# Optimization experiments

Hardware: AMD Instinct MI355X
Metric: run time of the kernel (lower is better)

The kernel has to match this reference:

```python
import jax, jax.numpy as jnp
import numpy as np

B, S, E, A = 4, 2048, 1024, 1024

def setup_inputs() -> dict:
    key = jax.random.key(0)
    ks = jax.random.split(key, 6)
    scale = 1.0 / np.sqrt(E)
    return {
        "query": jax.random.normal(ks[0], (B, S, E), jnp.float32),
        "key": jax.random.normal(ks[1], (B, S, E), jnp.float32),
        "value": jax.random.normal(ks[2], (B, S, E), jnp.float32),
        "Wq": jax.random.normal(ks[3], (E, A), jnp.float32) * scale,
        "bq": jnp.zeros((A,), jnp.float32),
        "Wk": jax.random.normal(ks[4], (E, A), jnp.float32) * scale,
        "bk": jnp.zeros((A,), jnp.float32),
        "Wv": jax.random.normal(ks[5], (E, A), jnp.float32) * scale,
        "bv": jnp.zeros((A,), jnp.float32),
    }

def reference(query, key, value, Wq, bq, Wk, bk, Wv, bv):
    # QKV linear projections: [B,S,E] @ [E,A] + [A]
    q = jnp.einsum("bse,ea->bsa", query, Wq) + bq
    k = jnp.einsum("bse,ea->bsa", key, Wk) + bk
    v = jnp.einsum("bse,ea->bsa", value, Wv) + bv
    # scaled dot-product attention (no mask, single head)
    inv_sqrt_d = 1.0 / jnp.sqrt(jnp.asarray(A, q.dtype))
    scores = jnp.einsum("bqa,bka->bqk", q, k) * inv_sqrt_d  # [B,S,S]
    probs = jax.nn.softmax(scores, axis=-1)
    return jnp.einsum("bqk,bka->bqa", probs, v)
```

## Files before the change

### kernel.cpp

```cpp
#include <hip/hip_runtime.h>

typedef unsigned short u16;
typedef __attribute__((ext_vector_type(4))) float f32x4;
typedef __attribute__((ext_vector_type(8))) short s16x8;
typedef __attribute__((ext_vector_type(8))) unsigned short u16x8;
typedef __attribute__((ext_vector_type(4))) unsigned short u16x4;

__device__ __forceinline__ u16 f2b(float x) {
  union { float f; unsigned u; } v; v.f = x;
  unsigned r = v.u + 0x7fffu + ((v.u >> 16) & 1u);
  return (u16)(r >> 16);
}
__device__ __forceinline__ float b2f(u16 x) {
  union { unsigned u; float f; } v; v.u = ((unsigned)x) << 16;
  return v.f;
}

__global__ __launch_bounds__(256) void cast3_f32_bf16(const float* __restrict__ s0,
                                                      const float* __restrict__ s1,
                                                      const float* __restrict__ s2,
                                                      u16* __restrict__ dst, long n4) {
  const float* src = (blockIdx.y == 0) ? s0 : ((blockIdx.y == 1) ? s1 : s2);
  long i = blockIdx.x * 256 + threadIdx.x;
  if (i >= n4) return;
  float4 f = ((const float4*)src)[i];
  u16x4 o;
  o.x = f2b(f.x); o.y = f2b(f.y); o.z = f2b(f.z); o.w = f2b(f.w);
  ((u16x4*)(dst + blockIdx.y * n4 * 4))[i] = o;
}

__global__ __launch_bounds__(256) void transpose_cast_w3(const float* __restrict__ w0,
                                                         const float* __restrict__ w1,
                                                         const float* __restrict__ w2,
                                                         u16* __restrict__ Wt, int E_, int A_) {
  __shared__ float tile[32][33];
  const float* W = (blockIdx.z == 0) ? w0 : ((blockIdx.z == 1) ? w1 : w2);
  u16* dst = Wt + (long)blockIdx.z * E_ * A_;
  int a0 = blockIdx.x * 32, e0 = blockIdx.y * 32;
  int tx = threadIdx.x & 31, ty = threadIdx.x >> 5;
  for (int i = ty; i < 32; i += 8) tile[i][tx] = W[(long)(e0 + i) * A_ + a0 + tx];
  __syncthreads();
  for (int i = ty; i < 32; i += 8) dst[(long)(a0 + i) * E_ + e0 + tx] = f2b(tile[tx][i]);
}

template<bool OUT_BF16>
__global__ __launch_bounds__(512, 2)
void gemm256(const u16* __restrict__ Ag, const u16* __restrict__ Bg,
             const float* __restrict__ b0, const float* __restrict__ b1,
             const float* __restrict__ b2, void* __restrict__ Cg,
             int gm, int K, int N, float scale,
             long sA, long sB, long sC,
             u16* __restrict__ VtG, long vtB, int vtS) {
  __shared__ u16 lds[65536];
  char* ldsc = (char*)lds;
  const int t = threadIdx.x;
  const int w = t >> 6, l = t & 63;
  const int wm = w >> 2, wn = w & 3;

  const int nwg = gridDim.x;
  const int Lb = blockIdx.x;
  const int chunk = nwg >> 3;
  const int id = (Lb & 7) * chunk + (Lb >> 3);
  const int im = id % gm, in = id / gm;
  const int m0 = im * 256, n0 = in * 256;
  const int z = blockIdx.z;
  const float* bias = (z == 0) ? b0 : ((z == 1) ? b1 : b2);

  const u16* Ab = Ag + (long)z * sA + (long)m0 * K;
  const u16* Bb = Bg + (long)z * sB + (long)n0 * K;

  const long so0 = (long)(w * 8 + (l >> 3)) * K + (long)(((l & 7) ^ (l >> 3)) << 3);
  const int ldst0 = w << 10;

  const int cb0 = ((l >> 4) ^ (l & 7)) << 4;
  const int arow = (l & 15) << 7;
  const int aoff0 = (wm << 14) + arow + cb0;
  const int aoff1 = aoff0 ^ 64;
  const int boff0 = 32768 + ((wn >> 1) << 14) + ((wn & 1) << 13) + arow + cb0;
  const int boff1 = boff0 ^ 64;

  f32x4 acc[8][4] = {};
  s16x8 af[4][2], bf[2][2];
  const int NT = K >> 6;
  const int NT2 = NT >> 1;

#define STG2(AB, KT) do {                                                                    \
    const u16* _sp = ((AB) ? Bb : Ab) + ((long)(KT) << 6) + so0;                             \
    const int _lo = (((KT) & 1) << 16) + ((AB) << 15) + ldst0;                               \
    _Pragma("unroll") for (int _h = 0; _h < 4; ++_h)                                         \
      __builtin_amdgcn_global_load_lds(                                                      \
          (const __attribute__((address_space(1))) unsigned int*)(_sp + (long)_h * 64 * K),  \
          (__attribute__((address_space(3))) unsigned int*)(ldsc + _lo + _h * 8192),         \
          16, 0, 0);                                                                         \
  } while (0)

#define PHASE(BUF, MH, NH, RDA_, RDB_, SAB, SKT, VMN) do {                                   \
    if (RDA_) {                                                                              \
      _Pragma("unroll") for (int i = 0; i < 4; ++i) {                                        \
        af[i][0] = *(const s16x8*)(ldsc + ((BUF) << 16) + ((MH) << 13) + (i << 11) + aoff0); \
        af[i][1] = *(const s16x8*)(ldsc + ((BUF) << 16) + ((MH) << 13) + (i << 11) + aoff1); \
      }                                                                                      \
    }                                                                                        \
    if (RDB_) {                                                                              \
      _Pragma("unroll") for (int j = 0; j < 2; ++j) {                                        \
        bf[j][0] = *(const s16x8*)(ldsc + ((BUF) << 16) + ((NH) << 12) + (j << 11) + boff0); \
        bf[j][1] = *(const s16x8*)(ldsc + ((BUF) << 16) + ((NH) << 12) + (j << 11) + boff1); \
      }                                                                                      \
    }                                                                                        \
    if ((SAB) == 0) STG2(0, SKT);                                                            \
    if ((SAB) == 1) STG2(1, SKT);                                                            \
    __builtin_amdgcn_s_setprio(1);                                                           \
    _Pragma("unroll") for (int kk = 0; kk < 2; ++kk)                                         \
      _Pragma("unroll") for (int i = 0; i < 4; ++i)                                          \
        _Pragma("unroll") for (int j = 0; j < 2; ++j)                                        \
          acc[(MH) * 4 + i][(NH) * 2 + j] = __builtin_amdgcn_mfma_f32_16x16x32_bf16(         \
              af[i][kk], bf[j][kk], acc[(MH) * 4 + i][(NH) * 2 + j], 0, 0, 0);               \
    __builtin_amdgcn_s_setprio(0);                                                           \
    if ((VMN) == 4) asm volatile("s_waitcnt vmcnt(4)" ::: "memory");                         \
    if ((VMN) == 0) asm volatile("s_waitcnt vmcnt(0)" ::: "memory");                         \
    __builtin_amdgcn_s_barrier();                                                            \
  } while (0)

  STG2(0, 0); STG2(1, 0); STG2(0, 1);
  asm volatile("s_waitcnt vmcnt(4)" ::: "memory");
  __builtin_amdgcn_s_barrier();

  for (int i2 = 0; i2 < NT2 - 1; ++i2) {
    const int kb = 2 * i2 + 1, kn = 2 * i2 + 2, kn1 = 2 * i2 + 3;
    PHASE(0, 0, 0, 1, 1, 1, kb, -1);
    PHASE(0, 0, 1, 0, 1, -1, 0, -1);
    PHASE(0, 1, 1, 1, 0, -1, 0, -1);
    PHASE(0, 1, 0, 0, 1, 0, kn, 4);
    PHASE(1, 0, 0, 1, 1, 1, kn, -1);
    PHASE(1, 0, 1, 0, 1, -1, 0, -1);
    PHASE(1, 1, 1, 1, 0, -1, 0, -1);
    PHASE(1, 1, 0, 0, 1, 0, kn1, 4);
  }
  {
    PHASE(0, 0, 0, 1, 1, 1, NT - 1, -1);
    PHASE(0, 0, 1, 0, 1, -1, 0, -1);
    PHASE(0, 1, 1, 1, 0, -1, 0, -1);
    PHASE(0, 1, 0, 0, 1, -1, 0, 0);
    PHASE(1, 0, 0, 1, 1, -1, 0, -1);
    PHASE(1, 0, 1, 0, 1, -1, 0, -1);
    PHASE(1, 1, 1, 1, 0, -1, 0, -1);
    PHASE(1, 1, 0, 0, 1, -1, 0, -1);
  }
#undef PHASE
#undef STG2

  float bj[4];
#pragma unroll
  for (int j = 0; j < 4; ++j) {
    int col = n0 + wn * 64 + j * 16 + (l & 15);
    bj[j] = bias ? bias[col] : 0.0f;
  }

  if (OUT_BF16 && VtG != nullptr && z == 2) {
    const int b = m0 / vtS, smod = m0 % vtS;
    u16* vbase = VtG + (long)b * vtB + smod + wm * 128 + ((l >> 4) << 2);
#pragma unroll
    for (int i8 = 0; i8 < 8; ++i8)
#pragma unroll
      for (int j = 0; j < 4; ++j) {
        int col = n0 + wn * 64 + j * 16 + (l & 15);
        u16x4 o;
#pragma unroll
        for (int r = 0; r < 4; ++r) o[r] = f2b(acc[i8][j][r] * scale + bj[j]);
        *(u16x4*)(vbase + (long)col * vtS + i8 * 16) = o;
      }
  } else {
    long rbase = (long)z * sC + (long)(m0 + wm * 128 + ((l >> 4) << 2)) * N + n0 + wn * 64 + (l & 15);
#pragma unroll
    for (int i8 = 0; i8 < 8; ++i8)
#pragma unroll
      for (int j = 0; j < 4; ++j)
#pragma unroll
        for (int r = 0; r < 4; ++r) {
          float v = acc[i8][j][r] * scale + bj[j];
          long ro = rbase + (long)(i8 * 16 + r) * N + j * 16;
          if (OUT_BF16) ((u16*)Cg)[ro] = f2b(v);
          else          ((float*)Cg)[ro] = v;
        }
  }
}

__device__ __forceinline__ float wred_max(float x) {
  for (int o = 32; o > 0; o >>= 1) x = fmaxf(x, __shfl_xor(x, o));
  return x;
}
__device__ __forceinline__ float wred_sum(float x) {
  for (int o = 32; o > 0; o >>= 1) x += __shfl_xor(x, o);
  return x;
}

__global__ __launch_bounds__(256) void softmax_rows_bf16(const u16* __restrict__ S,
                                                         u16* __restrict__ P, int ncols) {
  long row = blockIdx.x;
  const u16x8* s8 = (const u16x8*)(S + row * (long)ncols);
  int t = threadIdx.x;
  int wave = t >> 6, lane = t & 63;
  u16x8 a = s8[t];
  float f[8];
#pragma unroll
  for (int i = 0; i < 8; i++) f[i] = b2f(a[i]);
  float m = f[0];
#pragma unroll
  for (int i = 1; i < 8; i++) m = fmaxf(m, f[i]);
  m = wred_max(m);
  __shared__ float redm[4], reds[4];
  if (lane == 0) redm[wave] = m;
  __syncthreads();
  m = fmaxf(fmaxf(redm[0], redm[1]), fmaxf(redm[2], redm[3]));

  float e[8], s = 0.f;
#pragma unroll
  for (int i = 0; i < 8; i++) { e[i] = __expf(f[i] - m); s += e[i]; }
  s = wred_sum(s);
  if (lane == 0) reds[wave] = s;
  __syncthreads();
  s = reds[0] + reds[1] + reds[2] + reds[3];
  float inv = 1.0f / s;

  u16x8 o;
#pragma unroll
  for (int i = 0; i < 8; i++) o[i] = f2b(e[i] * inv);
  ((u16x8*)(P + row * (long)ncols))[t] = o;
}

extern "C" void kernel_launch(void* const* d_in, const int* in_sizes, int n_in,
                              void* d_out, int out_size, void* d_ws, size_t ws_size,
                              hipStream_t stream) {
  const float* query = (const float*)d_in[0];
  const float* key_  = (const float*)d_in[1];
  const float* value = (const float*)d_in[2];
  const float* Wq = (const float*)d_in[3];
  const float* bq = (const float*)d_in[4];
  const float* Wk = (const float*)d_in[5];
  const float* bk = (const float*)d_in[6];
  const float* Wv = (const float*)d_in[7];
  const float* bv = (const float*)d_in[8];

  constexpr int B = 4, S = 2048, E = 1024, A = 1024;
  constexpr long MB = 1024 * 1024;
  char* ws = (char*)d_ws;
  u16* Qb  = (u16*)(ws + 0 * MB);
  u16* Kb  = (u16*)(ws + 16 * MB);
  u16* Vt  = (u16*)(ws + 48 * MB);
  u16* P   = (u16*)(ws + 64 * MB);
  u16* Sc  = (u16*)(ws + 96 * MB);
  u16* Xq  = (u16*)(ws + 96 * MB);
  u16* WqT = (u16*)(ws + 144 * MB);

  const long n = (long)B * S * E;
  const long n4 = n / 4;
  dim3 blk(256);
  dim3 blk5(512);

  cast3_f32_bf16<<<dim3(n4 / 256, 3), blk, 0, stream>>>(query, key_, value, Xq, n4);

  transpose_cast_w3<<<dim3(A / 32, E / 32, 3), blk, 0, stream>>>(Wq, Wk, Wv, WqT, E, A);

  gemm256<true><<<dim3(128, 1, 3), blk5, 0, stream>>>(
      Xq, WqT, bq, bk, bv, Qb, 32, E, A, 1.0f,
      (long)8 * MB, (long)1 * MB, (long)8 * MB,
      Vt, (long)A * S, S);

  gemm256<true><<<dim3(64, 1, 4), blk5, 0, stream>>>(
      Qb, Kb, nullptr, nullptr, nullptr, Sc, 8, A, S, 0.03125f,
      (long)S * A, (long)S * A, (long)S * S, nullptr, 0, 1);

  softmax_rows_bf16<<<dim3(B * S), blk, 0, stream>>>(Sc, P, S);

  gemm256<false><<<dim3(32, 1, 4), blk5, 0, stream>>>(
      P, Vt, nullptr, nullptr, nullptr, (float*)d_out, 8, S, A, 1.0f,
      (long)S * S, (long)S * A, (long)S * A, nullptr, 0, 1);
}
```

Measured before the change: 322.6 us.

## Rework GEMM into K=32 four-stage pipeline with templated N tile

Replaces the two-buffer, K=64, eight-phase GEMM main loop with a four-buffer ring of K=32 tiles, prefetched three steps ahead. Each step runs two half-steps split across the M halves, with a new XOR swizzle. The N tile is now a template parameter, and the final PV GEMM uses 128-wide N tiles to launch twice as many workgroups. The block-to-tile mapping changes to row-major over N tiles. This aims for deeper load/compute overlap and better occupancy on the PV GEMM, at the cost of more barriers per unit of K and a riskier waitcnt schedule.

```diff
diff --git a/kernel.cpp b/kernel.cpp
--- a/kernel.cpp
+++ b/kernel.cpp
@@ -43,16 +43,20 @@
   for (int i = ty; i < 32; i += 8) dst[(long)(a0 + i) * E_ + e0 + tx] = f2b(tile[tx][i]);
 }
 
-template<bool OUT_BF16>
+template<int BN, bool OUT_BF16>
 __global__ __launch_bounds__(512, 2)
-void gemm256(const u16* __restrict__ Ag, const u16* __restrict__ Bg,
+void gemmK32(const u16* __restrict__ Ag, const u16* __restrict__ Bg,
              const float* __restrict__ b0, const float* __restrict__ b1,
              const float* __restrict__ b2, void* __restrict__ Cg,
-             int gm, int K, int N, float scale,
+             int gn, int K, int N, float scale,
              long sA, long sB, long sC,
              u16* __restrict__ VtG, long vtB, int vtS) {
-  __shared__ u16 lds[65536];
-  char* ldsc = (char*)lds;
+  constexpr int J = BN / 64;
+  constexpr int WN = BN / 4;
+  constexpr int OPS = 2 + BN / 128;
+  constexpr int BUFSZ = (256 + BN) * 64;
+  __shared__ __align__(128) char ldsc[4 * BUFSZ];
+
   const int t = threadIdx.x;
   const int w = t >> 6, l = t & 63;
   const int wm = w >> 2, wn = w & 3;
@@ -61,98 +65,94 @@
   const int Lb = blockIdx.x;
   const int chunk = nwg >> 3;
   const int id = (Lb & 7) * chunk + (Lb >> 3);
-  const int im = id % gm, in = id / gm;
-  const int m0 = im * 256, n0 = in * 256;
+  const int im = id / gn, in = id % gn;
+  const int m0 = im * 256, n0 = in * BN;
   const int z = blockIdx.z;
   const float* bias = (z == 0) ? b0 : ((z == 1) ? b1 : b2);
 
   const u16* Ab = Ag + (long)z * sA + (long)m0 * K;
   const u16* Bb = Bg + (long)z * sB + (long)n0 * K;
 
-  const long so0 = (long)(w * 8 + (l >> 3)) * K + (long)(((l & 7) ^ (l >> 3)) << 3);
-  const int ldst0 = w << 10;
-
-  const int cb0 = ((l >> 4) ^ (l & 7)) << 4;
-  const int arow = (l & 15) << 7;
-  const int aoff0 = (wm << 14) + arow + cb0;
-  const int aoff1 = aoff0 ^ 64;
-  const int boff0 = 32768 + ((wn >> 1) << 14) + ((wn & 1) << 13) + arow + cb0;
-  const int boff1 = boff0 ^ 64;
-
-  f32x4 acc[8][4] = {};
-  s16x8 af[4][2], bf[2][2];
-  const int NT = K >> 6;
-  const int NT2 = NT >> 1;
-
-#define STG2(AB, KT) do {                                                                    \
-    const u16* _sp = ((AB) ? Bb : Ab) + ((long)(KT) << 6) + so0;                             \
-    const int _lo = (((KT) & 1) << 16) + ((AB) << 15) + ldst0;                               \
-    _Pragma("unroll") for (int _h = 0; _h < 4; ++_h)                                         \
-      __builtin_amdgcn_global_load_lds(                                                      \
-          (const __attribute__((address_space(1))) unsigned int*)(_sp + (long)_h * 64 * K),  \
-          (__attribute__((address_space(3))) unsigned int*)(ldsc + _lo + _h * 8192),         \
-          16, 0, 0);                                                                         \
+  const long so0 = (long)(t >> 2) * K + (long)(((t & 3) ^ ((t >> 3) & 3)) << 3);
+  const int d16 = t * 16;
+
+  const int cbR = ((l >> 4) ^ ((l >> 1) & 3)) << 4;
+  const int aB = (wm << 13) + ((l & 15) << 6) + cbR;
+  const int bB = 16384 + wn * (WN * 64) + ((l & 15) << 6) + cbR;
+
+  f32x4 acc[8][J] = {};
+  s16x8 af[4], bf[J];
+  const int NTt = K >> 5;
+
+#define GLD(SRC, DST)                                                                        \
+  __builtin_amdgcn_global_load_lds(                                                         \
+      (const __attribute__((address_space(1))) unsigned int*)(SRC),                         \
+      (__attribute__((address_space(3))) unsigned int*)(DST), 16, 0, 0)
+
+#define STGA(TT) do {                                                                        \
+    const u16* _s = Ab + ((long)(TT) << 5) + so0;                                            \
+    char* _d = ldsc + ((TT) & 3) * BUFSZ + d16;                                              \
+    GLD(_s, _d);                                                                             \
+    GLD(_s + (long)128 * K, _d + 8192);                                                      \
   } while (0)
 
-#define PHASE(BUF, MH, NH, RDA_, RDB_, SAB, SKT, VMN) do {                                   \
-    if (RDA_) {                                                                              \
-      _Pragma("unroll") for (int i = 0; i < 4; ++i) {                                        \
-        af[i][0] = *(const s16x8*)(ldsc + ((BUF) << 16) + ((MH) << 13) + (i << 11) + aoff0); \
-        af[i][1] = *(const s16x8*)(ldsc + ((BUF) << 16) + ((MH) << 13) + (i << 11) + aoff1); \
-      }                                                                                      \
-    }                                                                                        \
-    if (RDB_) {                                                                              \
-      _Pragma("unroll") for (int j = 0; j < 2; ++j) {                                        \
-        bf[j][0] = *(const s16x8*)(ldsc + ((BUF) << 16) + ((NH) << 12) + (j << 11) + boff0); \
-        bf[j][1] = *(const s16x8*)(ldsc + ((BUF) << 16) + ((NH) << 12) + (j << 11) + boff1); \
-      }                                                                                      \
-    }                                                                                        \
-    if ((SAB) == 0) STG2(0, SKT);                                                            \
-    if ((SAB) == 1) STG2(1, SKT);                                                            \
-    __builtin_amdgcn_s_setprio(1);                                                           \
-    _Pragma("unroll") for (int kk = 0; kk < 2; ++kk)                                         \
-      _Pragma("unroll") for (int i = 0; i < 4; ++i)                                          \
-        _Pragma("unroll") for (int j = 0; j < 2; ++j)                                        \
-          acc[(MH) * 4 + i][(NH) * 2 + j] = __builtin_amdgcn_mfma_f32_16x16x32_bf16(         \
-              af[i][kk], bf[j][kk], acc[(MH) * 4 + i][(NH) * 2 + j], 0, 0, 0);               \
-    __builtin_amdgcn_s_setprio(0);                                                           \
-    if ((VMN) == 4) asm volatile("s_waitcnt vmcnt(4)" ::: "memory");                         \
-    if ((VMN) == 0) asm volatile("s_waitcnt vmcnt(0)" ::: "memory");                         \
-    __builtin_amdgcn_s_barrier();                                                            \
+#define STGB(TT) do {                                                                        \
+    const u16* _s = Bb + ((long)(TT) << 5) + so0;                                            \
+    char* _d = ldsc + ((TT) & 3) * BUFSZ + 16384 + d16;                                      \
+    GLD(_s, _d);                                                                             \
+    if (BN == 256) GLD(_s + (long)128 * K, _d + 8192);                                       \
   } while (0)
 
-  STG2(0, 0); STG2(1, 0); STG2(0, 1);
-  asm volatile("s_waitcnt vmcnt(4)" ::: "memory");
+  STGA(0); STGB(0); STGA(1); STGB(1); STGA(2); STGB(2);
+  if (OPS == 4) asm volatile("s_waitcnt vmcnt(8)" ::: "memory");
+  else          asm volatile("s_waitcnt vmcnt(6)" ::: "memory");
   __builtin_amdgcn_s_barrier();
 
-  for (int i2 = 0; i2 < NT2 - 1; ++i2) {
-    const int kb = 2 * i2 + 1, kn = 2 * i2 + 2, kn1 = 2 * i2 + 3;
-    PHASE(0, 0, 0, 1, 1, 1, kb, -1);
-    PHASE(0, 0, 1, 0, 1, -1, 0, -1);
-    PHASE(0, 1, 1, 1, 0, -1, 0, -1);
-    PHASE(0, 1, 0, 0, 1, 0, kn, 4);
-    PHASE(1, 0, 0, 1, 1, 1, kn, -1);
-    PHASE(1, 0, 1, 0, 1, -1, 0, -1);
-    PHASE(1, 1, 1, 1, 0, -1, 0, -1);
-    PHASE(1, 1, 0, 0, 1, 0, kn1, 4);
+  for (int tt = 0; tt < NTt; ++tt) {
+    const int base = (tt & 3) * BUFSZ;
+#pragma unroll
+    for (int i = 0; i < 4; ++i) af[i] = *(const s16x8*)(ldsc + base + aB + (i << 10));
+#pragma unroll
+    for (int j = 0; j < J; ++j) bf[j] = *(const s16x8*)(ldsc + base + bB + (j << 10));
+    if (tt + 3 < NTt) STGA(tt + 3);
+    __builtin_amdgcn_s_setprio(1);
+#pragma unroll
+    for (int i = 0; i < 4; ++i)
+#pragma unroll
+      for (int j = 0; j < J; ++j)
+        acc[i][j] = __builtin_amdgcn_mfma_f32_16x16x32_bf16(af[i], bf[j], acc[i][j], 0, 0, 0);
+    __builtin_amdgcn_s_setprio(0);
+    __builtin_amdgcn_s_barrier();
+
+#pragma unroll
+    for (int i = 0; i < 4; ++i) af[i] = *(const s16x8*)(ldsc + base + aB + 4096 + (i << 10));
+    if (tt + 3 < NTt) STGB(tt + 3);
+    __builtin_amdgcn_s_setprio(1);
+#pragma unroll
+    for (int i = 0; i < 4; ++i)
+#pragma unroll
+      for (int j = 0; j < J; ++j)
+        acc[4 + i][j] = __builtin_amdgcn_mfma_f32_16x16x32_bf16(af[i], bf[j], acc[4 + i][j], 0, 0, 0);
+    __builtin_amdgcn_s_setprio(0);
+    if (tt <= NTt - 4) {
+      if (OPS == 4) asm volatile("s_waitcnt vmcnt(8)" ::: "memory");
+      else          asm volatile("s_waitcnt vmcnt(6)" ::: "memory");
+    } else if (tt == NTt - 3) {
+      if (OPS == 4) asm volatile("s_waitcnt vmcnt(4)" ::: "memory");
+      else          asm volatile("s_waitcnt vmcnt(3)" ::: "memory");
+    } else if (tt == NTt - 2) {
+      asm volatile("s_waitcnt vmcnt(0)" ::: "memory");
+    }
+    __builtin_amdgcn_s_barrier();
   }
-  {
-    PHASE(0, 0, 0, 1, 1, 1, NT - 1, -1);
-    PHASE(0, 0, 1, 0, 1, -1, 0, -1);
-    PHASE(0, 1, 1, 1, 0, -1, 0, -1);
-    PHASE(0, 1, 0, 0, 1, -1, 0, 0);
-    PHASE(1, 0, 0, 1, 1, -1, 0, -1);
-    PHASE(1, 0, 1, 0, 1, -1, 0, -1);
-    PHASE(1, 1, 1, 1, 0, -1, 0, -1);
-    PHASE(1, 1, 0, 0, 1, -1, 0, -1);
-  }
-#undef PHASE
-#undef STG2
-
-  float bj[4];
-#pragma unroll
-  for (int j = 0; j < 4; ++j) {
-    int col = n0 + wn * 64 + j * 16 + (l & 15);
+#undef STGA
+#undef STGB
+#undef GLD
+
+  float bj[J];
+#pragma unroll
+  for (int j = 0; j < J; ++j) {
+    int col = n0 + wn * WN + j * 16 + (l & 15);
     bj[j] = bias ? bias[col] : 0.0f;
   }
 
@@ -162,19 +162,19 @@
 #pragma unroll
     for (int i8 = 0; i8 < 8; ++i8)
 #pragma unroll
-      for (int j = 0; j < 4; ++j) {
-        int col = n0 + wn * 64 + j * 16 + (l & 15);
+      for (int j = 0; j < J; ++j) {
+        int col = n0 + wn * WN + j * 16 + (l & 15);
         u16x4 o;
 #pragma unroll
         for (int r = 0; r < 4; ++r) o[r] = f2b(acc[i8][j][r] * scale + bj[j]);
         *(u16x4*)(vbase + (long)col * vtS + i8 * 16) = o;
       }
   } else {
-    long rbase = (long)z * sC + (long)(m0 + wm * 128 + ((l >> 4) << 2)) * N + n0 + wn * 64 + (l & 15);
+    long rbase = (long)z * sC + (long)(m0 + wm * 128 + ((l >> 4) << 2)) * N + n0 + wn * WN + (l & 15);
 #pragma unroll
     for (int i8 = 0; i8 < 8; ++i8)
 #pragma unroll
-      for (int j = 0; j < 4; ++j)
+      for (int j = 0; j < J; ++j)
 #pragma unroll
         for (int r = 0; r < 4; ++r) {
           float v = acc[i8][j][r] * scale + bj[j];
@@ -255,24 +255,23 @@
   const long n = (long)B * S * E;
   const long n4 = n / 4;
   dim3 blk(256);
-  dim3 blk5(512);
 
   cast3_f32_bf16<<<dim3(n4 / 256, 3), blk, 0, stream>>>(query, key_, value, Xq, n4);
 
   transpose_cast_w3<<<dim3(A / 32, E / 32, 3), blk, 0, stream>>>(Wq, Wk, Wv, WqT, E, A);
 
-  gemm256<true><<<dim3(128, 1, 3), blk5, 0, stream>>>(
-      Xq, WqT, bq, bk, bv, Qb, 32, E, A, 1.0f,
+  gemmK32<256, true><<<dim3(128, 1, 3), dim3(512), 0, stream>>>(
+      Xq, WqT, bq, bk, bv, Qb, 4, E, A, 1.0f,
       (long)8 * MB, (long)1 * MB, (long)8 * MB,
       Vt, (long)A * S, S);
 
-  gemm256<true><<<dim3(64, 1, 4), blk5, 0, stream>>>(
+  gemmK32<256, true><<<dim3(64, 1, 4), dim3(512), 0, stream>>>(
       Qb, Kb, nullptr, nullptr, nullptr, Sc, 8, A, S, 0.03125f,
       (long)S * A, (long)S * A, (long)S * S, nullptr, 0, 1);
 
   softmax_rows_bf16<<<dim3(B * S), blk, 0, stream>>>(Sc, P, S);
 
-  gemm256<false><<<dim3(32, 1, 4), blk5, 0, stream>>>(
+  gemmK32<128, false><<<dim3(64, 1, 4), dim3(512), 0, stream>>>(
       P, Vt, nullptr, nullptr, nullptr, (float*)d_out, 8, S, A, 1.0f,
       (long)S * S, (long)S * A, (long)S * A, nullptr, 0, 1);
 }
```

Result: faster. 312.9 us (-3.0%).
